# Kernel optimization log

Measured on AMD Instinct MI355X. Metric: run time of the kernel, lower is better.

Reference implementation:

```python
import jax, jax.numpy as jnp
import numpy as np
from jax import lax

W = 28
H = 28
EPS = 1e-5


def _k(x):
    return jax.nn.relu(1.0 - jnp.abs(x))


def _wireframe(x_in):
    # x_in: (B, E, 3); p = x_in[...,0]; theta = x_in[...,1:3] scaled by (W,H)
    p = x_in[:, :, 0]
    theta = x_in[:, :, 1:3] * jnp.asarray([W, H], dtype=x_in.dtype)
    gx = jnp.arange(W, dtype=x_in.dtype)[:, None]  # grid x varies along rows
    gy = jnp.arange(H, dtype=x_in.dtype)[None, :]  # grid y varies along cols
    tx = theta[:, :, 0][:, :, None, None]
    ty = theta[:, :, 1][:, :, None, None]
    F = _k(gx - tx) * _k(gy - ty)               # (B, E, W, H)
    I = jnp.max(p[:, :, None, None] * F, axis=1)  # (B, W, H)
    return I[:, None, :, :]                      # (B, 1, W, H)


def _conv(x, w, b):
    y = lax.conv_general_dilated(x, w, window_strides=(1, 1), padding='SAME',
                                 dimension_numbers=('NCHW', 'OIHW', 'NCHW'))
    return y + b[None, :, None, None]


def _bn_train(x, gamma, beta):
    # training-mode BatchNorm2d: batch statistics over (N,H,W), biased var
    mean = jnp.mean(x, axis=(0, 2, 3), keepdims=True)
    var = jnp.mean(jnp.square(x - mean), axis=(0, 2, 3), keepdims=True)
    xn = (x - mean) * lax.rsqrt(var + EPS)
    return xn * gamma[None, :, None, None] + beta[None, :, None, None]


def _pool2(x):
    B, C, Hh, Ww = x.shape
    return x.reshape(B, C, Hh // 2, 2, Ww // 2, 2).max(axis=(3, 5))


def setup_inputs() -> dict:
    key = jax.random.key(0)
    ks = jax.random.split(key, 12)
    B, E = 128, 512
    std = 0.02
    return {
        'x_in': jax.random.uniform(ks[0], (B, E, 3), dtype=jnp.float32),
        'conv1_w': std * jax.random.normal(ks[1], (4, 1, 3, 3), jnp.float32),
        'conv1_b': jnp.zeros((4,), jnp.float32),
        'bn1_g': jnp.ones((4,), jnp.float32),
        'bn1_b': jnp.zeros((4,), jnp.float32),
        'conv2_w': std * jax.random.normal(ks[2], (8, 4, 3, 3), jnp.float32),
        'conv2_b': jnp.zeros((8,), jnp.float32),
        'bn2_g': jnp.ones((8,), jnp.float32),
        'bn2_b': jnp.zeros((8,), jnp.float32),
        'conv3_w': std * jax.random.normal(ks[3], (16, 8, 3, 3), jnp.float32),
        'conv3_b': jnp.zeros((16,), jnp.float32),
        'bn3_g': jnp.ones((16,), jnp.float32),
        'bn3_b': jnp.zeros((16,), jnp.float32),
        'fc1_w': std * jax.random.normal(ks[4], (128, 16 * 7 * 7), jnp.float32),
        'fc1_b': jnp.zeros((128,), jnp.float32),
        'fc2_w': std * jax.random.normal(ks[5], (1, 128), jnp.float32),
        'fc2_b': jnp.zeros((1,), jnp.float32),
    }


def reference(x_in, conv1_w, conv1_b, bn1_g, bn1_b, conv2_w, conv2_b, bn2_g, bn2_b,
              conv3_w, conv3_b, bn3_g, bn3_b, fc1_w, fc1_b, fc2_w, fc2_b):
    x = _wireframe(x_in)                                   # (B,1,28,28)
    x = _pool2(jax.nn.relu(_bn_train(_conv(x, conv1_w, conv1_b), bn1_g, bn1_b)))   # (B,4,14,14)
    x = _pool2(jax.nn.relu(_bn_train(_conv(x, conv2_w, conv2_b), bn2_g, bn2_b)))   # (B,8,7,7)
    x = jax.nn.relu(_bn_train(_conv(x, conv3_w, conv3_b), bn3_g, bn3_b))           # (B,16,7,7)
    x = x.reshape(x.shape[0], -1)                          # (B,784)
    x = jax.nn.relu(x @ fc1_w.T + fc1_b)
    x = x @ fc2_w.T + fc2_b                                # (B,1)
    return x.mean(0).reshape(1)
```

## Files before the change

### kernel.cpp

```cpp
#include <hip/hip_runtime.h>
#include <math.h>

#define EPSV 1e-5f

__device__ __forceinline__ float dot4(float4 a, float4 b) {
    return a.x * b.x + a.y * b.y + a.z * b.z + a.w * b.w;
}

__device__ __forceinline__ void st_rlx(float* p, float v) {
    __hip_atomic_store(p, v, __ATOMIC_RELAXED, __HIP_MEMORY_SCOPE_AGENT);
}
__device__ __forceinline__ float ld_rlx(const float* p) {
    return __hip_atomic_load(p, __ATOMIC_RELAXED, __HIP_MEMORY_SCOPE_AGENT);
}
__device__ __forceinline__ void stu_rlx(unsigned* p, unsigned v) {
    __hip_atomic_store(p, v, __ATOMIC_RELAXED, __HIP_MEMORY_SCOPE_AGENT);
}
__device__ __forceinline__ unsigned ldu_rlx(const unsigned* p) {
    return __hip_atomic_load(p, __ATOMIC_RELAXED, __HIP_MEMORY_SCOPE_AGENT);
}

__device__ __forceinline__ void gbar(unsigned* flags, int stage, unsigned magic) {
    asm volatile("s_waitcnt vmcnt(0)" ::: "memory");
    __syncthreads();
    if (threadIdx.x == 0)
        stu_rlx(&flags[(stage << 7) + blockIdx.x], magic);
    if (threadIdx.x < 128) {
        while (ldu_rlx(&flags[(stage << 7) + threadIdx.x]) != magic)
            asm volatile("s_sleep 1" ::: "memory");
    }
    __syncthreads();
}

#define MAGIC0 0x13572468u
#define MAGIC1 0x13572469u
#define MAGIC2 0x1357246Au
#define MAGIC3 0x1357246Bu


__global__ __launch_bounds__(256) void k_fused(
    const float* __restrict__ x_in,
    const float* __restrict__ w1,  const float* __restrict__ b1,
    const float* __restrict__ g1,  const float* __restrict__ be1,
    const float* __restrict__ w2,  const float* __restrict__ b2,
    const float* __restrict__ g2,  const float* __restrict__ be2,
    const float* __restrict__ w3,  const float* __restrict__ b3,
    const float* __restrict__ g3,  const float* __restrict__ be3,
    const float* __restrict__ fc1w, const float* __restrict__ fc1b,
    const float* __restrict__ fc2w, const float* __restrict__ fc2b,
    unsigned* __restrict__ flags,
    float* __restrict__ pp1, float* __restrict__ pp2,
    float* __restrict__ pp3, float* __restrict__ pf,
    float* __restrict__ out)
{
    __shared__ __align__(16) float sxin[1536];
    __shared__ float sI[784];
    __shared__ float a1[4 * 784];
    __shared__ float p1s[4 * 196];
    __shared__ float a2[8 * 196];
    __shared__ float p2s[8 * 49];
    __shared__ float a3[16 * 49];
    __shared__ __align__(16) float sx[1024];
    __shared__ float sh[128];
    __shared__ float sw1[36], sw2[288], sw3[1152];
    __shared__ float scs[16], sfs[16];
    __shared__ double sred[32];

    const int tid  = threadIdx.x;
    const int lane = tid & 63;
    const int wv   = tid >> 6;
    const int b    = blockIdx.x;

    {
        const float4* src = (const float4*)x_in + (size_t)b * 384;
        float4* dst = (float4*)sxin;
        for (int i = tid; i < 384; i += 256) dst[i] = src[i];
    }
    for (int i = tid; i < 784;  i += 256) sI[i]  = 0.0f;
    for (int i = tid; i < 288;  i += 256) sw2[i] = w2[i];
    for (int i = tid; i < 1152; i += 256) sw3[i] = w3[i];
    if (tid < 36) sw1[tid] = w1[tid];
    __syncthreads();

    for (int e = tid; e < 512; e += 256) {
        float p  = sxin[e * 3];
        float tx = sxin[e * 3 + 1] * 28.0f;
        float ty = sxin[e * 3 + 2] * 28.0f;
        int x0 = (int)floorf(tx); float fx = tx - (float)x0;
        int y0 = (int)floorf(ty); float fy = ty - (float)y0;
        float kx[2] = {1.0f - fx, fx};
        float ky[2] = {1.0f - fy, fy};
        #pragma unroll
        for (int dx = 0; dx < 2; ++dx) {
            int gx = x0 + dx;
            if (gx < 0 || gx > 27) continue;
            #pragma unroll
            for (int dy = 0; dy < 2; ++dy) {
                int gy = y0 + dy;
                if (gy < 0 || gy > 27) continue;
                float v = p * (kx[dx] * ky[dy]);
                atomicMax((int*)&sI[gx * 28 + gy], __float_as_int(v));
            }
        }
    }
    __syncthreads();

    {
        const float bias = b1[wv];
        float ls = 0.0f, lq = 0.0f;
        for (int p = lane; p < 784; p += 64) {
            int i = p / 28, j = p % 28;
            float s = bias;
            #pragma unroll
            for (int a = 0; a < 3; ++a) {
                int ii = i + a - 1;
                if (ii < 0 || ii > 27) continue;
                #pragma unroll
                for (int c = 0; c < 3; ++c) {
                    int jj = j + c - 1;
                    if (jj < 0 || jj > 27) continue;
                    s += sw1[wv * 9 + a * 3 + c] * sI[ii * 28 + jj];
                }
            }
            a1[wv * 784 + p] = s;
            ls += s; lq += s * s;
        }
        #pragma unroll
        for (int off = 32; off; off >>= 1) {
            ls += __shfl_down(ls, off);
            lq += __shfl_down(lq, off);
        }
        if (lane == 0) {
            st_rlx(&pp1[wv * 128 + b],       ls);
            st_rlx(&pp1[(4 + wv) * 128 + b], lq);
        }
    }
    gbar(flags, 0, MAGIC0);

    {
        const int c = tid >> 5, k = tid & 31;
        double t = 0.0;
        #pragma unroll
        for (int j = 0; j < 4; ++j) t += (double)ld_rlx(&pp1[c * 128 + k + j * 32]);
        #pragma unroll
        for (int off = 16; off; off >>= 1) t += __shfl_xor(t, off);
        if (k == 0) sred[c] = t;
    }
    __syncthreads();
    if (tid < 4) {
        const double n = 128.0 * 784.0;
        double m = sred[tid] / n;
        double v = sred[4 + tid] / n - m * m;
        float scale = g1[tid] * rsqrtf((float)v + EPSV);
        scs[tid] = scale;
        sfs[tid] = be1[tid] - (float)m * scale;
    }
    __syncthreads();
    for (int idx = tid; idx < 784; idx += 256) {
        int c = idx / 196, pix = idx % 196;
        int r = pix / 14, col = pix % 14;
        const float* yb = a1 + c * 784;
        float scale = scs[c], shift = sfs[c];
        float v00 = yb[(2*r    )*28 + 2*col    ] * scale + shift;
        float v01 = yb[(2*r    )*28 + 2*col + 1] * scale + shift;
        float v10 = yb[(2*r + 1)*28 + 2*col    ] * scale + shift;
        float v11 = yb[(2*r + 1)*28 + 2*col + 1] * scale + shift;
        p1s[idx] = fmaxf(fmaxf(fmaxf(v00, v01), fmaxf(v10, v11)), 0.0f);
    }
    __syncthreads();

    {
        const int o = tid >> 5, l32 = tid & 31;
        const float bias = b2[o];
        float ls = 0.0f, lq = 0.0f;
        for (int p = l32; p < 196; p += 32) {
            int i = p / 14, j = p % 14;
            float s = bias;
            #pragma unroll
            for (int c = 0; c < 4; ++c) {
                #pragma unroll
                for (int a = 0; a < 3; ++a) {
                    int ii = i + a - 1;
                    if (ii < 0 || ii > 13) continue;
                    #pragma unroll
                    for (int d = 0; d < 3; ++d) {
                        int jj = j + d - 1;
                        if (jj < 0 || jj > 13) continue;
                        s += sw2[((o * 4 + c) * 3 + a) * 3 + d] * p1s[c * 196 + ii * 14 + jj];
                    }
                }
            }
            a2[o * 196 + p] = s;
            ls += s; lq += s * s;
        }
        #pragma unroll
        for (int off = 16; off; off >>= 1) {
            ls += __shfl_xor(ls, off);
            lq += __shfl_xor(lq, off);
        }
        if (l32 == 0) {
            st_rlx(&pp2[o * 128 + b],       ls);
            st_rlx(&pp2[(8 + o) * 128 + b], lq);
        }
    }
    gbar(flags, 1, MAGIC1);

    {
        const int c = tid >> 4, k = tid & 15;
        double t = 0.0;
        #pragma unroll
        for (int j = 0; j < 8; ++j) t += (double)ld_rlx(&pp2[c * 128 + k + j * 16]);
        #pragma unroll
        for (int off = 8; off; off >>= 1) t += __shfl_xor(t, off);
        if (k == 0) sred[c] = t;
    }
    __syncthreads();
    if (tid < 8) {
        const double n = 128.0 * 196.0;
        double m = sred[tid] / n;
        double v = sred[8 + tid] / n - m * m;
        float scale = g2[tid] * rsqrtf((float)v + EPSV);
        scs[tid] = scale;
        sfs[tid] = be2[tid] - (float)m * scale;
    }
    __syncthreads();
    for (int idx = tid; idx < 392; idx += 256) {
        int c = idx / 49, pix = idx % 49;
        int r = pix / 7, col = pix % 7;
        const float* yb = a2 + c * 196;
        float scale = scs[c], shift = sfs[c];
        float v00 = yb[(2*r    )*14 + 2*col    ] * scale + shift;
        float v01 = yb[(2*r    )*14 + 2*col + 1] * scale + shift;
        float v10 = yb[(2*r + 1)*14 + 2*col    ] * scale + shift;
        float v11 = yb[(2*r + 1)*14 + 2*col + 1] * scale + shift;
        p2s[idx] = fmaxf(fmaxf(fmaxf(v00, v01), fmaxf(v10, v11)), 0.0f);
    }
    __syncthreads();

    {
        const int o = tid >> 4, l16 = tid & 15;
        const float bias = b3[o];
        float ls = 0.0f, lq = 0.0f;
        for (int p = l16; p < 49; p += 16) {
            int i = p / 7, j = p % 7;
            float s = bias;
            #pragma unroll
            for (int c = 0; c < 8; ++c) {
                #pragma unroll
                for (int a = 0; a < 3; ++a) {
                    int ii = i + a - 1;
                    if (ii < 0 || ii > 6) continue;
                    #pragma unroll
                    for (int d = 0; d < 3; ++d) {
                        int jj = j + d - 1;
                        if (jj < 0 || jj > 6) continue;
                        s += sw3[((o * 8 + c) * 3 + a) * 3 + d] * p2s[c * 49 + ii * 7 + jj];
                    }
                }
            }
            a3[o * 49 + p] = s;
            ls += s; lq += s * s;
        }
        #pragma unroll
        for (int off = 8; off; off >>= 1) {
            ls += __shfl_xor(ls, off);
            lq += __shfl_xor(lq, off);
        }
        if (l16 == 0) {
            st_rlx(&pp3[o * 128 + b],        ls);
            st_rlx(&pp3[(16 + o) * 128 + b], lq);
        }
    }
    gbar(flags, 2, MAGIC2);

    {
        const int c = tid >> 3, k = tid & 7;
        double t = 0.0;
        #pragma unroll
        for (int j = 0; j < 16; ++j) t += (double)ld_rlx(&pp3[c * 128 + k + j * 8]);
        #pragma unroll
        for (int off = 4; off; off >>= 1) t += __shfl_xor(t, off);
        if (k == 0) sred[c] = t;
    }
    __syncthreads();
    if (tid < 16) {
        const double n = 128.0 * 49.0;
        double m = sred[tid] / n;
        double v = sred[16 + tid] / n - m * m;
        float scale = g3[tid] * rsqrtf((float)v + EPSV);
        scs[tid] = scale;
        sfs[tid] = be3[tid] - (float)m * scale;
    }
    __syncthreads();
    for (int i = tid; i < 1024; i += 256)
        sx[i] = (i < 784) ? fmaxf(a3[i] * scs[i / 49] + sfs[i / 49], 0.0f) : 0.0f;
    __syncthreads();

    {
        const float4* xr4 = (const float4*)sx;
        const float4 xa = xr4[lane];
        const float4 xb = xr4[64 + lane];
        const float4 xc = xr4[128 + lane];
        const float4 xd = xr4[192 + lane];
        const int jbase = wv * 32;
        for (int r0 = 0; r0 < 32; r0 += 4) {
            const float4* w0r = (const float4*)(fc1w + (size_t)(jbase + r0    ) * 784);
            const float4* w1r = (const float4*)(fc1w + (size_t)(jbase + r0 + 1) * 784);
            const float4* w2r = (const float4*)(fc1w + (size_t)(jbase + r0 + 2) * 784);
            const float4* w3r = (const float4*)(fc1w + (size_t)(jbase + r0 + 3) * 784);
            float s0 = dot4(w0r[lane], xa) + dot4(w0r[64+lane], xb) + dot4(w0r[128+lane], xc);
            float s1 = dot4(w1r[lane], xa) + dot4(w1r[64+lane], xb) + dot4(w1r[128+lane], xc);
            float s2 = dot4(w2r[lane], xa) + dot4(w2r[64+lane], xb) + dot4(w2r[128+lane], xc);
            float s3 = dot4(w3r[lane], xa) + dot4(w3r[64+lane], xb) + dot4(w3r[128+lane], xc);
            if (lane < 4) {
                s0 += dot4(w0r[192+lane], xd);
                s1 += dot4(w1r[192+lane], xd);
                s2 += dot4(w2r[192+lane], xd);
                s3 += dot4(w3r[192+lane], xd);
            }
            #pragma unroll
            for (int off = 32; off; off >>= 1) {
                s0 += __shfl_xor(s0, off);
                s1 += __shfl_xor(s1, off);
                s2 += __shfl_xor(s2, off);
                s3 += __shfl_xor(s3, off);
            }
            if (lane == 0) {
                sh[jbase + r0    ] = fmaxf(s0 + fc1b[jbase + r0    ], 0.0f);
                sh[jbase + r0 + 1] = fmaxf(s1 + fc1b[jbase + r0 + 1], 0.0f);
                sh[jbase + r0 + 2] = fmaxf(s2 + fc1b[jbase + r0 + 2], 0.0f);
                sh[jbase + r0 + 3] = fmaxf(s3 + fc1b[jbase + r0 + 3], 0.0f);
            }
        }
    }
    __syncthreads();

    if (tid < 64) {
        float v = sh[tid] * fc2w[tid] + sh[tid + 64] * fc2w[tid + 64];
        #pragma unroll
        for (int off = 32; off; off >>= 1) v += __shfl_xor(v, off);
        if (tid == 0) st_rlx(&pf[b], v);
    }
    asm volatile("s_waitcnt vmcnt(0)" ::: "memory");
    __syncthreads();
    if (tid == 0) stu_rlx(&flags[(3 << 7) + b], MAGIC3);
    if (b != 0) return;

    if (tid < 128) {
        while (ldu_rlx(&flags[(3 << 7) + tid]) != MAGIC3)
            asm volatile("s_sleep 1" ::: "memory");
    }
    __syncthreads();
    if (tid < 64) {
        float v = ld_rlx(&pf[tid]) + ld_rlx(&pf[tid + 64]);
        #pragma unroll
        for (int off = 32; off; off >>= 1) v += __shfl_xor(v, off);
        if (tid == 0) out[0] = v * (1.0f / 128.0f) + fc2b[0];
    }
}

extern "C" void kernel_launch(void* const* d_in, const int* in_sizes, int n_in,
                              void* d_out, int out_size, void* d_ws, size_t ws_size,
                              hipStream_t stream) {
    const float* x_in  = (const float*)d_in[0];
    const float* w1    = (const float*)d_in[1];
    const float* b1    = (const float*)d_in[2];
    const float* g1    = (const float*)d_in[3];
    const float* be1   = (const float*)d_in[4];
    const float* w2    = (const float*)d_in[5];
    const float* b2    = (const float*)d_in[6];
    const float* g2    = (const float*)d_in[7];
    const float* be2   = (const float*)d_in[8];
    const float* w3    = (const float*)d_in[9];
    const float* b3    = (const float*)d_in[10];
    const float* g3    = (const float*)d_in[11];
    const float* be3   = (const float*)d_in[12];
    const float* fc1w  = (const float*)d_in[13];
    const float* fc1b  = (const float*)d_in[14];
    const float* fc2w  = (const float*)d_in[15];
    const float* fc2b  = (const float*)d_in[16];

    float* ws  = (float*)d_ws;
    unsigned* flags = (unsigned*)ws;
    float* pp1 = ws + 512;
    float* pp2 = ws + 1536;
    float* pp3 = ws + 3584;
    float* pf  = ws + 7680;
    float* out = (float*)d_out;

    hipMemsetAsync(flags, 0, 512 * sizeof(unsigned), stream);

    void* args[] = {
        (void*)&x_in,
        (void*)&w1, (void*)&b1, (void*)&g1, (void*)&be1,
        (void*)&w2, (void*)&b2, (void*)&g2, (void*)&be2,
        (void*)&w3, (void*)&b3, (void*)&g3, (void*)&be3,
        (void*)&fc1w, (void*)&fc1b, (void*)&fc2w, (void*)&fc2b,
        (void*)&flags, (void*)&pp1, (void*)&pp2, (void*)&pp3, (void*)&pf,
        (void*)&out
    };
    hipLaunchKernel((void*)k_fused, dim3(128), dim3(256), args, 0, stream);
}
```

Baseline: 140.2 us.

## Process four samples per block with 32 blocks to cut grid-barrier and fc1 weight traffic

The grid shrinks from 128 blocks (one sample each) to 32 blocks that each process four samples in sequence. Activations for all four samples stay in LDS between stages, so each software grid barrier waits on 32 flags instead of 128. In fc1, each loaded weight row is reused across four samples, and an early prefetch warms the L2 with a slice of fc1 weights and inputs. The cost is less parallelism: each block does four times the serial conv work, uses more LDS and holds more registers.

```diff
diff --git a/kernel.cpp b/kernel.cpp
--- a/kernel.cpp
+++ b/kernel.cpp
@@ -2,6 +2,8 @@
 #include <math.h>
 
 #define EPSV 1e-5f
+#define NB   32
+#define IT   4
 
 __device__ __forceinline__ float dot4(float4 a, float4 b) {
     return a.x * b.x + a.y * b.y + a.z * b.z + a.w * b.w;
@@ -24,9 +26,9 @@
     asm volatile("s_waitcnt vmcnt(0)" ::: "memory");
     __syncthreads();
     if (threadIdx.x == 0)
-        stu_rlx(&flags[(stage << 7) + blockIdx.x], magic);
-    if (threadIdx.x < 128) {
-        while (ldu_rlx(&flags[(stage << 7) + threadIdx.x]) != magic)
+        stu_rlx(&flags[(stage << 5) + blockIdx.x], magic);
+    if (threadIdx.x < NB) {
+        while (ldu_rlx(&flags[(stage << 5) + threadIdx.x]) != magic)
             asm volatile("s_sleep 1" ::: "memory");
     }
     __syncthreads();
@@ -50,64 +52,79 @@
     const float* __restrict__ fc2w, const float* __restrict__ fc2b,
     unsigned* __restrict__ flags,
     float* __restrict__ pp1, float* __restrict__ pp2,
-    float* __restrict__ pp3, float* __restrict__ pf,
+    float* __restrict__ pp3, float* __restrict__ pfb,
     float* __restrict__ out)
 {
     __shared__ __align__(16) float sxin[1536];
     __shared__ float sI[784];
-    __shared__ float a1[4 * 784];
-    __shared__ float p1s[4 * 196];
-    __shared__ float a2[8 * 196];
-    __shared__ float p2s[8 * 49];
-    __shared__ float a3[16 * 49];
-    __shared__ __align__(16) float sx[1024];
-    __shared__ float sh[128];
+    __shared__ float a1[IT][3136];
+    __shared__ float p1s[784];
+    __shared__ float a2[IT][1568];
+    __shared__ float p2s[392];
+    __shared__ float a3[IT][784];
+    __shared__ __align__(16) float sx4[IT][1024];
+    __shared__ float sh4[IT][128];
     __shared__ float sw1[36], sw2[288], sw3[1152];
     __shared__ float scs[16], sfs[16];
     __shared__ double sred[32];
+    __shared__ float spf[IT];
 
     const int tid  = threadIdx.x;
     const int lane = tid & 63;
     const int wv   = tid >> 6;
-    const int b    = blockIdx.x;
-
-    {
-        const float4* src = (const float4*)x_in + (size_t)b * 384;
-        float4* dst = (float4*)sxin;
-        for (int i = tid; i < 384; i += 256) dst[i] = src[i];
-    }
-    for (int i = tid; i < 784;  i += 256) sI[i]  = 0.0f;
+    const int bb   = blockIdx.x;
+
     for (int i = tid; i < 288;  i += 256) sw2[i] = w2[i];
     for (int i = tid; i < 1152; i += 256) sw3[i] = w3[i];
     if (tid < 36) sw1[tid] = w1[tid];
-    __syncthreads();
-
-    for (int e = tid; e < 512; e += 256) {
-        float p  = sxin[e * 3];
-        float tx = sxin[e * 3 + 1] * 28.0f;
-        float ty = sxin[e * 3 + 2] * 28.0f;
-        int x0 = (int)floorf(tx); float fx = tx - (float)x0;
-        int y0 = (int)floorf(ty); float fy = ty - (float)y0;
-        float kx[2] = {1.0f - fx, fx};
-        float ky[2] = {1.0f - fy, fy};
-        #pragma unroll
-        for (int dx = 0; dx < 2; ++dx) {
-            int gx = x0 + dx;
-            if (gx < 0 || gx > 27) continue;
-            #pragma unroll
-            for (int dy = 0; dy < 2; ++dy) {
-                int gy = y0 + dy;
-                if (gy < 0 || gy > 27) continue;
-                float v = p * (kx[dx] * ky[dy]);
-                atomicMax((int*)&sI[gx * 28 + gy], __float_as_int(v));
-            }
-        }
-    }
-    __syncthreads();
-
-    {
+    {
+        const float4* wp = (const float4*)(fc1w + (size_t)bb * 3136);
+        for (int i = tid; i < 784; i += 256) {
+            float4 t = wp[i];
+            asm volatile("" :: "v"(t.x), "v"(t.y), "v"(t.z), "v"(t.w));
+        }
+    }
+    {
+        const float4* xp = (const float4*)x_in + (size_t)bb * IT * 384;
+        for (int i = tid; i < IT * 384; i += 256) {
+            float4 t = xp[i];
+            asm volatile("" :: "v"(t.x), "v"(t.y), "v"(t.z), "v"(t.w));
+        }
+    }
+
+    float ls1 = 0.0f, lq1 = 0.0f;
+    for (int it = 0; it < IT; ++it) {
+        __syncthreads();
+        for (int i = tid; i < 784; i += 256) sI[i] = 0.0f;
+        {
+            const float4* src = (const float4*)x_in + ((size_t)bb * IT + it) * 384;
+            float4* dst = (float4*)sxin;
+            for (int i = tid; i < 384; i += 256) dst[i] = src[i];
+        }
+        __syncthreads();
+        for (int e = tid; e < 512; e += 256) {
+            float p  = sxin[e * 3];
+            float tx = sxin[e * 3 + 1] * 28.0f;
+            float ty = sxin[e * 3 + 2] * 28.0f;
+            int x0 = (int)floorf(tx); float fx = tx - (float)x0;
+            int y0 = (int)floorf(ty); float fy = ty - (float)y0;
+            float kx[2] = {1.0f - fx, fx};
+            float ky[2] = {1.0f - fy, fy};
+            #pragma unroll
+            for (int dx = 0; dx < 2; ++dx) {
+                int gx = x0 + dx;
+                if (gx < 0 || gx > 27) continue;
+                #pragma unroll
+                for (int dy = 0; dy < 2; ++dy) {
+                    int gy = y0 + dy;
+                    if (gy < 0 || gy > 27) continue;
+                    float v = p * (kx[dx] * ky[dy]);
+                    atomicMax((int*)&sI[gx * 28 + gy], __float_as_int(v));
+                }
+            }
+        }
+        __syncthreads();
         const float bias = b1[wv];
-        float ls = 0.0f, lq = 0.0f;
         for (int p = lane; p < 784; p += 64) {
             int i = p / 28, j = p % 28;
             float s = bias;
@@ -122,26 +139,24 @@
                     s += sw1[wv * 9 + a * 3 + c] * sI[ii * 28 + jj];
                 }
             }
-            a1[wv * 784 + p] = s;
-            ls += s; lq += s * s;
-        }
-        #pragma unroll
-        for (int off = 32; off; off >>= 1) {
-            ls += __shfl_down(ls, off);
-            lq += __shfl_down(lq, off);
-        }
-        if (lane == 0) {
-            st_rlx(&pp1[wv * 128 + b],       ls);
-            st_rlx(&pp1[(4 + wv) * 128 + b], lq);
-        }
+            a1[it][wv * 784 + p] = s;
+            ls1 += s; lq1 += s * s;
+        }
+    }
+    #pragma unroll
+    for (int off = 32; off; off >>= 1) {
+        ls1 += __shfl_down(ls1, off);
+        lq1 += __shfl_down(lq1, off);
+    }
+    if (lane == 0) {
+        st_rlx(&pp1[wv * NB + bb],       ls1);
+        st_rlx(&pp1[(4 + wv) * NB + bb], lq1);
     }
     gbar(flags, 0, MAGIC0);
 
     {
         const int c = tid >> 5, k = tid & 31;
-        double t = 0.0;
-        #pragma unroll
-        for (int j = 0; j < 4; ++j) t += (double)ld_rlx(&pp1[c * 128 + k + j * 32]);
+        double t = (double)ld_rlx(&pp1[c * NB + k]);
         #pragma unroll
         for (int off = 16; off; off >>= 1) t += __shfl_xor(t, off);
         if (k == 0) sred[c] = t;
@@ -156,23 +171,22 @@
         sfs[tid] = be1[tid] - (float)m * scale;
     }
     __syncthreads();
-    for (int idx = tid; idx < 784; idx += 256) {
-        int c = idx / 196, pix = idx % 196;
-        int r = pix / 14, col = pix % 14;
-        const float* yb = a1 + c * 784;
-        float scale = scs[c], shift = sfs[c];
-        float v00 = yb[(2*r    )*28 + 2*col    ] * scale + shift;
-        float v01 = yb[(2*r    )*28 + 2*col + 1] * scale + shift;
-        float v10 = yb[(2*r + 1)*28 + 2*col    ] * scale + shift;
-        float v11 = yb[(2*r + 1)*28 + 2*col + 1] * scale + shift;
-        p1s[idx] = fmaxf(fmaxf(fmaxf(v00, v01), fmaxf(v10, v11)), 0.0f);
-    }
-    __syncthreads();
-
-    {
-        const int o = tid >> 5, l32 = tid & 31;
-        const float bias = b2[o];
-        float ls = 0.0f, lq = 0.0f;
+    float ls2 = 0.0f, lq2 = 0.0f;
+    const int o2 = tid >> 5, l32 = tid & 31;
+    for (int it = 0; it < IT; ++it) {
+        for (int idx = tid; idx < 784; idx += 256) {
+            int c = idx / 196, pix = idx % 196;
+            int r = pix / 14, col = pix % 14;
+            const float* yb = a1[it] + c * 784;
+            float scale = scs[c], shift = sfs[c];
+            float v00 = yb[(2*r    )*28 + 2*col    ] * scale + shift;
+            float v01 = yb[(2*r    )*28 + 2*col + 1] * scale + shift;
+            float v10 = yb[(2*r + 1)*28 + 2*col    ] * scale + shift;
+            float v11 = yb[(2*r + 1)*28 + 2*col + 1] * scale + shift;
+            p1s[idx] = fmaxf(fmaxf(fmaxf(v00, v01), fmaxf(v10, v11)), 0.0f);
+        }
+        __syncthreads();
+        const float bias = b2[o2];
         for (int p = l32; p < 196; p += 32) {
             int i = p / 14, j = p % 14;
             float s = bias;
@@ -186,30 +200,30 @@
                     for (int d = 0; d < 3; ++d) {
                         int jj = j + d - 1;
                         if (jj < 0 || jj > 13) continue;
-                        s += sw2[((o * 4 + c) * 3 + a) * 3 + d] * p1s[c * 196 + ii * 14 + jj];
+                        s += sw2[((o2 * 4 + c) * 3 + a) * 3 + d] * p1s[c * 196 + ii * 14 + jj];
                     }
                 }
             }
-            a2[o * 196 + p] = s;
-            ls += s; lq += s * s;
-        }
-        #pragma unroll
-        for (int off = 16; off; off >>= 1) {
-            ls += __shfl_xor(ls, off);
-            lq += __shfl_xor(lq, off);
-        }
-        if (l32 == 0) {
-            st_rlx(&pp2[o * 128 + b],       ls);
-            st_rlx(&pp2[(8 + o) * 128 + b], lq);
-        }
+            a2[it][o2 * 196 + p] = s;
+            ls2 += s; lq2 += s * s;
+        }
+        __syncthreads();
+    }
+    #pragma unroll
+    for (int off = 16; off; off >>= 1) {
+        ls2 += __shfl_xor(ls2, off);
+        lq2 += __shfl_xor(lq2, off);
+    }
+    if (l32 == 0) {
+        st_rlx(&pp2[o2 * NB + bb],       ls2);
+        st_rlx(&pp2[(8 + o2) * NB + bb], lq2);
     }
     gbar(flags, 1, MAGIC1);
 
     {
         const int c = tid >> 4, k = tid & 15;
-        double t = 0.0;
-        #pragma unroll
-        for (int j = 0; j < 8; ++j) t += (double)ld_rlx(&pp2[c * 128 + k + j * 16]);
+        double t = (double)ld_rlx(&pp2[c * NB + k])
+                 + (double)ld_rlx(&pp2[c * NB + k + 16]);
         #pragma unroll
         for (int off = 8; off; off >>= 1) t += __shfl_xor(t, off);
         if (k == 0) sred[c] = t;
@@ -224,23 +238,22 @@
         sfs[tid] = be2[tid] - (float)m * scale;
     }
     __syncthreads();
-    for (int idx = tid; idx < 392; idx += 256) {
-        int c = idx / 49, pix = idx % 49;
-        int r = pix / 7, col = pix % 7;
-        const float* yb = a2 + c * 196;
-        float scale = scs[c], shift = sfs[c];
-        float v00 = yb[(2*r    )*14 + 2*col    ] * scale + shift;
-        float v01 = yb[(2*r    )*14 + 2*col + 1] * scale + shift;
-        float v10 = yb[(2*r + 1)*14 + 2*col    ] * scale + shift;
-        float v11 = yb[(2*r + 1)*14 + 2*col + 1] * scale + shift;
-        p2s[idx] = fmaxf(fmaxf(fmaxf(v00, v01), fmaxf(v10, v11)), 0.0f);
-    }
-    __syncthreads();
-
-    {
-        const int o = tid >> 4, l16 = tid & 15;
-        const float bias = b3[o];
-        float ls = 0.0f, lq = 0.0f;
+    float ls3 = 0.0f, lq3 = 0.0f;
+    const int o3 = tid >> 4, l16 = tid & 15;
+    for (int it = 0; it < IT; ++it) {
+        for (int idx = tid; idx < 392; idx += 256) {
+            int c = idx / 49, pix = idx % 49;
+            int r = pix / 7, col = pix % 7;
+            const float* yb = a2[it] + c * 196;
+            float scale = scs[c], shift = sfs[c];
+            float v00 = yb[(2*r    )*14 + 2*col    ] * scale + shift;
+            float v01 = yb[(2*r    )*14 + 2*col + 1] * scale + shift;
+            float v10 = yb[(2*r + 1)*14 + 2*col    ] * scale + shift;
+            float v11 = yb[(2*r + 1)*14 + 2*col + 1] * scale + shift;
+            p2s[idx] = fmaxf(fmaxf(fmaxf(v00, v01), fmaxf(v10, v11)), 0.0f);
+        }
+        __syncthreads();
+        const float bias = b3[o3];
         for (int p = l16; p < 49; p += 16) {
             int i = p / 7, j = p % 7;
             float s = bias;
@@ -254,22 +267,23 @@
                     for (int d = 0; d < 3; ++d) {
                         int jj = j + d - 1;
                         if (jj < 0 || jj > 6) continue;
-                        s += sw3[((o * 8 + c) * 3 + a) * 3 + d] * p2s[c * 49 + ii * 7 + jj];
+                        s += sw3[((o3 * 8 + c) * 3 + a) * 3 + d] * p2s[c * 49 + ii * 7 + jj];
                     }
                 }
             }
-            a3[o * 49 + p] = s;
-            ls += s; lq += s * s;
-        }
-        #pragma unroll
-        for (int off = 8; off; off >>= 1) {
-            ls += __shfl_xor(ls, off);
-            lq += __shfl_xor(lq, off);
-        }
-        if (l16 == 0) {
-            st_rlx(&pp3[o * 128 + b],        ls);
-            st_rlx(&pp3[(16 + o) * 128 + b], lq);
-        }
+            a3[it][o3 * 49 + p] = s;
+            ls3 += s; lq3 += s * s;
+        }
+        __syncthreads();
+    }
+    #pragma unroll
+    for (int off = 8; off; off >>= 1) {
+        ls3 += __shfl_xor(ls3, off);
+        lq3 += __shfl_xor(lq3, off);
+    }
+    if (l16 == 0) {
+        st_rlx(&pp3[o3 * NB + bb],        ls3);
+        st_rlx(&pp3[(16 + o3) * NB + bb], lq3);
     }
     gbar(flags, 2, MAGIC2);
 
@@ -277,7 +291,7 @@
         const int c = tid >> 3, k = tid & 7;
         double t = 0.0;
         #pragma unroll
-        for (int j = 0; j < 16; ++j) t += (double)ld_rlx(&pp3[c * 128 + k + j * 8]);
+        for (int j = 0; j < 4; ++j) t += (double)ld_rlx(&pp3[c * NB + k + j * 8]);
         #pragma unroll
         for (int off = 4; off; off >>= 1) t += __shfl_xor(t, off);
         if (k == 0) sred[c] = t;
@@ -292,69 +306,84 @@
         sfs[tid] = be3[tid] - (float)m * scale;
     }
     __syncthreads();
-    for (int i = tid; i < 1024; i += 256)
-        sx[i] = (i < 784) ? fmaxf(a3[i] * scs[i / 49] + sfs[i / 49], 0.0f) : 0.0f;
-    __syncthreads();
-
-    {
-        const float4* xr4 = (const float4*)sx;
-        const float4 xa = xr4[lane];
-        const float4 xb = xr4[64 + lane];
-        const float4 xc = xr4[128 + lane];
-        const float4 xd = xr4[192 + lane];
+    for (int idx = tid; idx < IT * 1024; idx += 256) {
+        int i = idx >> 10, j = idx & 1023;
+        sx4[i][j] = (j < 784) ? fmaxf(a3[i][j] * scs[j / 49] + sfs[j / 49], 0.0f) : 0.0f;
+    }
+    __syncthreads();
+
+    {
+        float4 xA[IT], xB[IT], xC[IT], xD[IT];
+        #pragma unroll
+        for (int i = 0; i < IT; ++i) {
+            const float4* xr = (const float4*)sx4[i];
+            xA[i] = xr[lane]; xB[i] = xr[64 + lane];
+            xC[i] = xr[128 + lane]; xD[i] = xr[192 + lane];
+        }
         const int jbase = wv * 32;
-        for (int r0 = 0; r0 < 32; r0 += 4) {
-            const float4* w0r = (const float4*)(fc1w + (size_t)(jbase + r0    ) * 784);
-            const float4* w1r = (const float4*)(fc1w + (size_t)(jbase + r0 + 1) * 784);
-            const float4* w2r = (const float4*)(fc1w + (size_t)(jbase + r0 + 2) * 784);
-            const float4* w3r = (const float4*)(fc1w + (size_t)(jbase + r0 + 3) * 784);
-            float s0 = dot4(w0r[lane], xa) + dot4(w0r[64+lane], xb) + dot4(w0r[128+lane], xc);
-            float s1 = dot4(w1r[lane], xa) + dot4(w1r[64+lane], xb) + dot4(w1r[128+lane], xc);
-            float s2 = dot4(w2r[lane], xa) + dot4(w2r[64+lane], xb) + dot4(w2r[128+lane], xc);
-            float s3 = dot4(w3r[lane], xa) + dot4(w3r[64+lane], xb) + dot4(w3r[128+lane], xc);
+        for (int r0 = 0; r0 < 32; r0 += 2) {
+            const int j0 = jbase + r0, j1 = j0 + 1;
+            const float4* w0r = (const float4*)(fc1w + (size_t)j0 * 784);
+            const float4* w1r = (const float4*)(fc1w + (size_t)j1 * 784);
+            float4 w0a = w0r[lane], w0b = w0r[64 + lane], w0c = w0r[128 + lane];
+            float4 w1a = w1r[lane], w1b = w1r[64 + lane], w1c = w1r[128 + lane];
+            float s0[IT], s1[IT];
+            #pragma unroll
+            for (int i = 0; i < IT; ++i) {
+                s0[i] = dot4(w0a, xA[i]) + dot4(w0b, xB[i]) + dot4(w0c, xC[i]);
+                s1[i] = dot4(w1a, xA[i]) + dot4(w1b, xB[i]) + dot4(w1c, xC[i]);
+            }
             if (lane < 4) {
-                s0 += dot4(w0r[192+lane], xd);
-                s1 += dot4(w1r[192+lane], xd);
-                s2 += dot4(w2r[192+lane], xd);
-                s3 += dot4(w3r[192+lane], xd);
+                float4 w0d = w0r[192 + lane], w1d = w1r[192 + lane];
+                #pragma unroll
+                for (int i = 0; i < IT; ++i) {
+                    s0[i] += dot4(w0d, xD[i]);
+                    s1[i] += dot4(w1d, xD[i]);
+                }
             }
             #pragma unroll
             for (int off = 32; off; off >>= 1) {
-                s0 += __shfl_xor(s0, off);
-                s1 += __shfl_xor(s1, off);
-                s2 += __shfl_xor(s2, off);
-                s3 += __shfl_xor(s3, off);
+                #pragma unroll
+                for (int i = 0; i < IT; ++i) {
+                    s0[i] += __shfl_xor(s0[i], off);
+                    s1[i] += __shfl_xor(s1[i], off);
+                }
             }
             if (lane == 0) {
-                sh[jbase + r0    ] = fmaxf(s0 + fc1b[jbase + r0    ], 0.0f);
-                sh[jbase + r0 + 1] = fmaxf(s1 + fc1b[jbase + r0 + 1], 0.0f);
-                sh[jbase + r0 + 2] = fmaxf(s2 + fc1b[jbase + r0 + 2], 0.0f);
-                sh[jbase + r0 + 3] = fmaxf(s3 + fc1b[jbase + r0 + 3], 0.0f);
-            }
-        }
-    }
-    __syncthreads();
-
-    if (tid < 64) {
-        float v = sh[tid] * fc2w[tid] + sh[tid + 64] * fc2w[tid + 64];
+                float b0 = fc1b[j0], b1v = fc1b[j1];
+                #pragma unroll
+                for (int i = 0; i < IT; ++i) {
+                    sh4[i][j0] = fmaxf(s0[i] + b0,  0.0f);
+                    sh4[i][j1] = fmaxf(s1[i] + b1v, 0.0f);
+                }
+            }
+        }
+    }
+    __syncthreads();
+
+    {
+        float v = sh4[wv][lane] * fc2w[lane] + sh4[wv][64 + lane] * fc2w[64 + lane];
         #pragma unroll
         for (int off = 32; off; off >>= 1) v += __shfl_xor(v, off);
-        if (tid == 0) st_rlx(&pf[b], v);
-    }
+        if (lane == 0) spf[wv] = v;
+    }
+    __syncthreads();
+    if (tid == 0)
+        st_rlx(&pfb[bb], spf[0] + spf[1] + spf[2] + spf[3]);
     asm volatile("s_waitcnt vmcnt(0)" ::: "memory");
     __syncthreads();
-    if (tid == 0) stu_rlx(&flags[(3 << 7) + b], MAGIC3);
-    if (b != 0) return;
-
-    if (tid < 128) {
-        while (ldu_rlx(&flags[(3 << 7) + tid]) != MAGIC3)
+    if (tid == 0) stu_rlx(&flags[(3 << 5) + bb], MAGIC3);
+    if (bb != 0) return;
+
+    if (tid < NB) {
+        while (ldu_rlx(&flags[(3 << 5) + tid]) != MAGIC3)
             asm volatile("s_sleep 1" ::: "memory");
     }
     __syncthreads();
-    if (tid < 64) {
-        float v = ld_rlx(&pf[tid]) + ld_rlx(&pf[tid + 64]);
-        #pragma unroll
-        for (int off = 32; off; off >>= 1) v += __shfl_xor(v, off);
+    if (tid < NB) {
+        float v = ld_rlx(&pfb[tid]);
+        #pragma unroll
+        for (int off = 16; off; off >>= 1) v += __shfl_xor(v, off);
         if (tid == 0) out[0] = v * (1.0f / 128.0f) + fc2b[0];
     }
 }
@@ -382,13 +411,13 @@
 
     float* ws  = (float*)d_ws;
     unsigned* flags = (unsigned*)ws;
-    float* pp1 = ws + 512;
-    float* pp2 = ws + 1536;
-    float* pp3 = ws + 3584;
-    float* pf  = ws + 7680;
+    float* pp1 = ws + 128;
+    float* pp2 = ws + 384;
+    float* pp3 = ws + 896;
+    float* pfb = ws + 1920;
     float* out = (float*)d_out;
 
-    hipMemsetAsync(flags, 0, 512 * sizeof(unsigned), stream);
+    hipMemsetAsync(flags, 0, 128 * sizeof(unsigned), stream);
 
     void* args[] = {
         (void*)&x_in,
@@ -396,8 +425,8 @@
         (void*)&w2, (void*)&b2, (void*)&g2, (void*)&be2,
         (void*)&w3, (void*)&b3, (void*)&g3, (void*)&be3,
         (void*)&fc1w, (void*)&fc1b, (void*)&fc2w, (void*)&fc2b,
-        (void*)&flags, (void*)&pp1, (void*)&pp2, (void*)&pp3, (void*)&pf,
+        (void*)&flags, (void*)&pp1, (void*)&pp2, (void*)&pp3, (void*)&pfb,
         (void*)&out
     };
-    hipLaunchKernel((void*)k_fused, dim3(128), dim3(256), args, 0, stream);
-}
+    hipLaunchKernel((void*)k_fused, dim3(NB), dim3(256), args, 0, stream);
+}
```

New measurement: 239.2 us. 70.6% more time.
